# Performance work log

Hardware: AMD Instinct MI355X
Metric: run time of the kernel (lower is better)

## Reference

```python
import jax, jax.numpy as jnp
import numpy as np

H_DIM = 256
NUM_HEADS = 8
HEAD_DIM = H_DIM // NUM_HEADS
BN_EPS = 1e-5
SCALE = float(np.sqrt(HEAD_DIM))


def _lens():
    # 512 graphs, ragged vertex counts cycling 32/64/96/128 -> 40960 total rows
    return np.tile(np.array([32, 64, 96, 128], dtype=np.int64), 128)


def _pad(x, lens):
    # gather ragged rows of x [total, D] into padded [B, Lmax, D]; mask [B, Lmax]
    B = lens.shape[0]
    L = int(lens.max())
    off = np.zeros(B, np.int64)
    off[1:] = np.cumsum(lens)[:-1]
    pos = np.arange(L)
    idx = off[:, None] + np.minimum(pos[None, :], lens[:, None] - 1)
    mask = pos[None, :] < lens[:, None]
    return x[jnp.asarray(idx)], jnp.asarray(mask)


def _flat_idx(lens):
    # (graph_id, position) for every real row, to un-pad back to ragged layout
    b = np.repeat(np.arange(lens.shape[0]), lens)
    i = np.concatenate([np.arange(int(l)) for l in lens])
    return jnp.asarray(b), jnp.asarray(i)


def _forward(src_h, dst_h, src_lens, dst_lens,
             W1, b1, gamma1, beta1, W2, b2, gamma2, beta2):
    src_pad, src_mask = _pad(src_h, src_lens)   # [B, Ls, H]
    dst_pad, _ = _pad(dst_h, dst_lens)          # [B, Ld, H]
    B, Ls, _ = src_pad.shape
    Ld = dst_pad.shape[1]
    # NOTE: original torch code zips self.proj but never applies it, so
    # q = raw dst, k = v = raw src.  The .view(1, head_dim, heads, N) on the
    # channel-major tensor splits feature f as f = d*NUM_HEADS + h.
    q = dst_pad.reshape(B, Ld, HEAD_DIM, NUM_HEADS)
    k = src_pad.reshape(B, Ls, HEAD_DIM, NUM_HEADS)
    v = k
    scores = jnp.einsum('bndh,bmdh->bhnm', q, k) / SCALE
    scores = jnp.where(src_mask[:, None, None, :], scores, jnp.float32(-1e30))
    attn = jax.nn.softmax(scores, axis=-1)
    out = jnp.einsum('bhnm,bmdh->bndh', attn, v).reshape(B, Ld, H_DIM)
    bidx, iidx = _flat_idx(dst_lens)
    h_msg = out[bidx, iidx]                     # [total_dst, H] ragged again
    h = dst_h
    z = jnp.concatenate([h, h_msg], axis=-1)    # [N, 2H]
    y = z @ W1.T + b1
    y = gamma1 * (y - y.mean(0)) * jax.lax.rsqrt(y.var(0) + BN_EPS) + beta1
    y = jax.nn.relu(y)
    y = y @ W2.T + b2
    y = gamma2 * (y - y.mean(0)) * jax.lax.rsqrt(y.var(0) + BN_EPS) + beta2
    return h + y


def setup_inputs() -> dict:
    lens = _lens()
    N = int(lens.sum())
    ks = jax.random.split(jax.random.key(0), 4)
    return {
        'src_h': jax.random.normal(ks[0], (N, H_DIM), jnp.float32),
        'dst_h': jax.random.normal(ks[1], (N, H_DIM), jnp.float32),
        'src_num_verts': jnp.asarray(lens, jnp.int32),
        'dst_num_verts': jnp.asarray(lens, jnp.int32),
        'W1': jax.random.normal(ks[2], (H_DIM, 2 * H_DIM), jnp.float32) / np.float32(np.sqrt(2 * H_DIM)),
        'b1': jnp.zeros((H_DIM,), jnp.float32),
        'gamma1': jnp.ones((H_DIM,), jnp.float32),
        'beta1': jnp.zeros((H_DIM,), jnp.float32),
        'W2': jax.random.normal(ks[3], (H_DIM, H_DIM), jnp.float32) / np.float32(np.sqrt(H_DIM)),
        'b2': jnp.zeros((H_DIM,), jnp.float32),
        'gamma2': jnp.ones((H_DIM,), jnp.float32),
        'beta2': jnp.zeros((H_DIM,), jnp.float32),
    }


def reference(src_h, dst_h, src_num_verts, dst_num_verts,
              W1, b1, gamma1, beta1, W2, b2, gamma2, beta2):
    # segment lengths are static metadata (torch.split takes a Python list)
    src_lens = np.asarray(jax.device_get(src_num_verts), np.int64)
    dst_lens = np.asarray(jax.device_get(dst_num_verts), np.int64)
    return _forward(src_h, dst_h, src_lens, dst_lens,
                    W1, b1, gamma1, beta1, W2, b2, gamma2, beta2)
```

## Files before the change

### kernel.cpp

```cpp
#include <hip/hip_runtime.h>
#include <cstddef>

#define H 256
#define NHEADS 8
#define HD 32

typedef __attribute__((ext_vector_type(8))) short bf16x8;
typedef __attribute__((ext_vector_type(4))) float f32x4;

__device__ __forceinline__ float bf2f(unsigned short s) {
    unsigned u = ((unsigned)s) << 16; return __builtin_bit_cast(float, u);
}
__device__ __forceinline__ float bfe2f(short s) {
    unsigned u = ((unsigned)(unsigned short)s) << 16; return __builtin_bit_cast(float, u);
}
__device__ __forceinline__ unsigned short f2bf(float x) {
    unsigned u = __builtin_bit_cast(unsigned, x);
    u += 0x7fffu + ((u >> 16) & 1u);
    return (unsigned short)(u >> 16);
}
__device__ __forceinline__ void gl_lds16(const void* g, void* l) {
    __builtin_amdgcn_global_load_lds(
        (const __attribute__((address_space(1))) void*)g,
        (__attribute__((address_space(3))) void*)l, 16, 0, 0);
}

#define PS 2696
__global__ __launch_bounds__(256) void pre_kernel(
    const float* __restrict__ src, const float* __restrict__ dst,
    const float* __restrict__ W1, const float* __restrict__ W2,
    const int* __restrict__ slen, const int* __restrict__ dlen,
    unsigned short* __restrict__ KT, unsigned short* __restrict__ QT,
    unsigned short* __restrict__ W1p, unsigned short* __restrict__ W2bf,
    int* __restrict__ soff, int* __restrict__ doff,
    float* __restrict__ stats, int N, int B)
{
    __shared__ unsigned short pl[8 * PS];
    const int t = threadIdx.x;
    const int bid = blockIdx.x;
    const int prepB = N >> 5;

    if (bid < prepB) {
        const int rb = (bid >> 1) * 64;
        const int isrc = (bid & 1) == 0;
        const float* __restrict__ in = isrc ? src : dst;
        unsigned short* __restrict__ T = isrc ? KT : QT;
        #pragma unroll
        for (int i = 0; i < 16; ++i) {
            const int idx = t + i * 256;
            const int row = idx >> 6, f4 = idx & 63;
            const float4 v = ((const float4*)in)[(size_t)(rb + row) * 64 + f4];
            const int f0 = f4 * 4, h0 = f0 & 7, d = f0 >> 3;
            pl[(h0 + 0) * PS + row * 42 + d] = f2bf(v.x);
            pl[(h0 + 1) * PS + row * 42 + d] = f2bf(v.y);
            pl[(h0 + 2) * PS + row * 42 + d] = f2bf(v.z);
            pl[(h0 + 3) * PS + row * 42 + d] = f2bf(v.w);
        }
        __syncthreads();
        #pragma unroll
        for (int i = 0; i < 8; ++i) {
            const int idx = t + i * 256;
            const int h = idx >> 8, rem = idx & 255, row = rem >> 2, c = rem & 3;
            const bf16x8 val = *(const bf16x8*)&pl[h * PS + row * 42 + c * 8];
            *(bf16x8*)&T[(size_t)(h * N + rb + row) * 32 + c * 8] = val;
        }
    } else if (bid < prepB + 768) {
        const int idx = (bid - prepB) * 256 + t;
        if (idx < 131072) {
            const int kp = idx & 511, c = idx >> 9;
            const int half = kp >> 8, r = kp & 255, hh = r >> 5, d = r & 31;
            W1p[(size_t)c * 512 + kp] = f2bf(W1[(size_t)c * 512 + half * 256 + d * 8 + hh]);
        } else {
            const int i2 = idx - 131072;
            W2bf[i2] = f2bf(W2[i2]);
        }
    } else {
        stats[t] = 0.f; stats[t + 256] = 0.f; stats[t + 512] = 0.f; stats[t + 768] = 0.f;
        if (t < 64) {
            int sv[8], dv[8];
            int sl = 0, dl = 0;
            #pragma unroll
            for (int j = 0; j < 8; ++j) {
                const int g = t * 8 + j;
                sv[j] = sl; dv[j] = dl;
                sl += (g < B) ? slen[g] : 0;
                dl += (g < B) ? dlen[g] : 0;
            }
            int sx = sl, dx = dl;
            #pragma unroll
            for (int o = 1; o < 64; o <<= 1) {
                const int sy = __shfl_up(sx, o);
                const int dy = __shfl_up(dx, o);
                if (t >= o) { sx += sy; dx += dy; }
            }
            const int sbase = sx - sl, dbase = dx - dl;
            #pragma unroll
            for (int j = 0; j < 8; ++j) {
                const int g = t * 8 + j;
                if (g < B) { soff[g] = sbase + sv[j]; doff[g] = dbase + dv[j]; }
            }
        }
    }
}

template<int LS>
__device__ __forceinline__ void attn_body(
    const unsigned short* __restrict__ KT, const unsigned short* __restrict__ QT,
    unsigned short* __restrict__ OT,
    unsigned short* __restrict__ Ps, int N, int so, int df, int Ld, int h, int lane)
{
    constexpr int MT = LS / 16, CH = LS / 32;
    const int lr = lane & 15, lq = lane >> 4;
    const float iscale = 0.17677669529663687f;

    bf16x8 kf[MT];
    #pragma unroll
    for (int mt = 0; mt < MT; ++mt)
        kf[mt] = *(const bf16x8*)&KT[(size_t)(h * N + so + mt * 16 + lr) * 32 + lq * 8];

    bf16x8 vf[CH][2];
    #pragma unroll
    for (int c = 0; c < CH; ++c) {
        #pragma unroll
        for (int hf = 0; hf < 2; ++hf) {
            const bf16x8 kv = kf[2 * c + hf];
            const int nn = hf * 16 + lr;
            #pragma unroll
            for (int k = 0; k < 8; ++k)
                Ps[(lq * 8 + k) * 33 + nn] = (unsigned short)kv[k];
        }
        __asm__ volatile("" ::: "memory");
        __builtin_amdgcn_wave_barrier();
        #pragma unroll
        for (int dt = 0; dt < 2; ++dt)
            vf[c][dt] = *(const bf16x8*)&Ps[(dt * 16 + lr) * 33 + lq * 8];
        __asm__ volatile("" ::: "memory");
        __builtin_amdgcn_wave_barrier();
    }

    const int NT = Ld >> 4;
    bf16x8 qf = *(const bf16x8*)&QT[(size_t)(h * N + df + lr) * 32 + lq * 8];
    for (int nt = 0; nt < NT; ++nt) {
        bf16x8 qn = qf;
        if (nt + 1 < NT)
            qn = *(const bf16x8*)&QT[(size_t)(h * N + df + (nt + 1) * 16 + lr) * 32 + lq * 8];
        f32x4 s[MT];
        __builtin_amdgcn_s_setprio(1);
        #pragma unroll
        for (int mt = 0; mt < MT; ++mt) {
            f32x4 z = {0.f, 0.f, 0.f, 0.f};
            s[mt] = __builtin_amdgcn_mfma_f32_16x16x32_bf16(kf[mt], qf, z, 0, 0, 0);
        }
        __builtin_amdgcn_s_setprio(0);
        float mx = -INFINITY;
        #pragma unroll
        for (int mt = 0; mt < MT; ++mt)
            mx = fmaxf(mx, fmaxf(fmaxf(s[mt][0], s[mt][1]), fmaxf(s[mt][2], s[mt][3])));
        mx = fmaxf(mx, __shfl_xor(mx, 16));
        mx = fmaxf(mx, __shfl_xor(mx, 32));
        const float mxi = mx * iscale;
        float sum = 0.f;
        #pragma unroll
        for (int mt = 0; mt < MT; ++mt) {
            #pragma unroll
            for (int r = 0; r < 4; ++r) {
                const float e = __expf(s[mt][r] * iscale - mxi);
                s[mt][r] = e; sum += e;
            }
        }
        sum += __shfl_xor(sum, 16);
        sum += __shfl_xor(sum, 32);
        const float rinv = 1.f / sum;
        #pragma unroll
        for (int mt = 0; mt < MT; ++mt) {
            uint2 p;
            p.x = ((unsigned)f2bf(s[mt][0])) | (((unsigned)f2bf(s[mt][1])) << 16);
            p.y = ((unsigned)f2bf(s[mt][2])) | (((unsigned)f2bf(s[mt][3])) << 16);
            *(uint2*)&Ps[lr * 136 + mt * 16 + lq * 4] = p;
        }
        __asm__ volatile("" ::: "memory");
        __builtin_amdgcn_wave_barrier();
        f32x4 o0 = {0.f, 0.f, 0.f, 0.f}, o1 = {0.f, 0.f, 0.f, 0.f};
        __builtin_amdgcn_s_setprio(1);
        #pragma unroll
        for (int c = 0; c < CH; ++c) {
            const bf16x8 pa = *(const bf16x8*)&Ps[lr * 136 + c * 32 + lq * 8];
            o0 = __builtin_amdgcn_mfma_f32_16x16x32_bf16(pa, vf[c][0], o0, 0, 0, 0);
            o1 = __builtin_amdgcn_mfma_f32_16x16x32_bf16(pa, vf[c][1], o1, 0, 0, 0);
        }
        __builtin_amdgcn_s_setprio(0);
        __asm__ volatile("" ::: "memory");
        __builtin_amdgcn_wave_barrier();
        #pragma unroll
        for (int r = 0; r < 4; ++r) {
            const float rv = __shfl(rinv, lq * 4 + r);
            const int row = df + nt * 16 + lq * 4 + r;
            OT[(size_t)(h * N + row) * 32 + lr]      = f2bf(o0[r] * rv);
            OT[(size_t)(h * N + row) * 32 + 16 + lr] = f2bf(o1[r] * rv);
        }
        qf = qn;
    }
}

__global__ __launch_bounds__(256) void attn_mfma(
    const unsigned short* __restrict__ KT, const unsigned short* __restrict__ QT,
    unsigned short* __restrict__ OT,
    const int* __restrict__ soff, const int* __restrict__ doff,
    const int* __restrict__ slen, const int* __restrict__ dlen, int N)
{
    __shared__ unsigned short Ps[4][16 * 136];
    const int i = blockIdx.x >> 1, half = blockIdx.x & 1;
    const int grp = i >> 7, j = i & 127;
    const int b = 4 * j + (3 - grp);
    const int w = threadIdx.x >> 6, lane = threadIdx.x & 63;
    const int h = half * 4 + w;
    const int Ls = slen[b], Ld = dlen[b], so = soff[b], df = doff[b];
    switch (Ls) {
        case 32:  attn_body<32> (KT, QT, OT, Ps[w], N, so, df, Ld, h, lane); break;
        case 64:  attn_body<64> (KT, QT, OT, Ps[w], N, so, df, Ld, h, lane); break;
        case 96:  attn_body<96> (KT, QT, OT, Ps[w], N, so, df, Ld, h, lane); break;
        default:  attn_body<128>(KT, QT, OT, Ps[w], N, so, df, Ld, h, lane); break;
    }
}

__global__ __launch_bounds__(256) void gemm1_mfma(
    const unsigned short* __restrict__ QT, const unsigned short* __restrict__ OT,
    const unsigned short* __restrict__ W, const float* __restrict__ bias,
    unsigned short* __restrict__ out, float* __restrict__ sum, float* __restrict__ sq,
    int N)
{
    __shared__ unsigned short Abuf[2][8 * 512];
    __shared__ unsigned short Bbuf[2][8 * 512];
    const int tid = threadIdx.x;
    const int w = tid >> 6, lane = tid & 63;
    const int bid = blockIdx.x;
    const int xcd = bid & 7, q = bid >> 3;
    const int cb = q & 1, y = (q >> 1) * 8 + xcd;
    const int rowBase = y * 128, colBase = cb * 128;
    const int lr = lane & 15, lq = lane >> 4;
    const int wm = w >> 1, wn = w & 1;

    f32x4 acc[4][4];
    #pragma unroll
    for (int i = 0; i < 4; ++i)
        #pragma unroll
        for (int j = 0; j < 4; ++j) { f32x4 z = {0.f, 0.f, 0.f, 0.f}; acc[i][j] = z; }

    auto stage = [&](int ks, int bi) {
        const unsigned short* __restrict__ Ap = (ks < 8) ? QT : OT;
        const int hh = ks & 7;
        #pragma unroll
        for (int s = 0; s < 2; ++s) {
            const int sub = 2 * w + s;
            gl_lds16(Ap + (size_t)(hh * N + rowBase + sub * 16 + lr) * 32 + lq * 8,
                     &Abuf[bi][sub * 512]);
            gl_lds16(W + (size_t)(colBase + sub * 16 + lr) * 512 + ks * 32 + lq * 8,
                     &Bbuf[bi][sub * 512]);
        }
    };
    auto compute = [&](int bi) {
        bf16x8 af[4], bfr[4];
        #pragma unroll
        for (int i = 0; i < 4; ++i) af[i] = *(const bf16x8*)&Abuf[bi][(wm * 4 + i) * 512 + lane * 8];
        #pragma unroll
        for (int j = 0; j < 4; ++j) bfr[j] = *(const bf16x8*)&Bbuf[bi][(wn * 4 + j) * 512 + lane * 8];
        #pragma unroll
        for (int i = 0; i < 4; ++i)
            #pragma unroll
            for (int j = 0; j < 4; ++j)
                acc[i][j] = __builtin_amdgcn_mfma_f32_16x16x32_bf16(af[i], bfr[j], acc[i][j], 0, 0, 0);
    };

    stage(0, 0);
    __syncthreads();
    for (int ks = 0; ks < 16; ks += 2) {
        stage(ks + 1, 1);
        compute(0);
        __syncthreads();
        if (ks + 2 < 16) stage(ks + 2, 0);
        compute(1);
        __syncthreads();
    }

    const int col0 = colBase + wn * 64;
    #pragma unroll
    for (int j = 0; j < 4; ++j) {
        const int col = col0 + j * 16 + lr;
        const float bv = bias[col];
        float cs = 0.f, cq = 0.f;
        #pragma unroll
        for (int i = 0; i < 4; ++i) {
            const int row0 = rowBase + wm * 64 + i * 16 + lq * 4;
            #pragma unroll
            for (int r = 0; r < 4; ++r) {
                const float v = acc[i][j][r] + bv;
                cs += v; cq += v * v;
                out[(size_t)(row0 + r) * 256 + col] = f2bf(v);
            }
        }
        cs += __shfl_xor(cs, 16); cs += __shfl_xor(cs, 32);
        cq += __shfl_xor(cq, 16); cq += __shfl_xor(cq, 32);
        if (lq == 0) { atomicAdd(&sum[col], cs); atomicAdd(&sq[col], cq); }
    }
}

__global__ __launch_bounds__(256) void gemm2_fused(
    const unsigned short* __restrict__ y1,
    const unsigned short* __restrict__ W, const float* __restrict__ bias,
    const float* __restrict__ sum1, const float* __restrict__ sq1,
    const float* __restrict__ gamma1, const float* __restrict__ beta1,
    unsigned short* __restrict__ out, float* __restrict__ sum, float* __restrict__ sq,
    float invN)
{
    __shared__ unsigned short Abuf[2][8 * 512];
    __shared__ unsigned short Bbuf[2][8 * 512];
    __shared__ float scs[256], shs[256];
    const int tid = threadIdx.x;
    const int w = tid >> 6, lane = tid & 63;
    const int bid = blockIdx.x;
    const int xcd = bid & 7, q = bid >> 3;
    const int cb = q & 1, y = (q >> 1) * 8 + xcd;
    const int rowBase = y * 128, colBase = cb * 128;
    const int lr = lane & 15, lq = lane >> 4;
    const int wm = w >> 1, wn = w & 1;

    {
        const float mean = sum1[tid] * invN;
        const float var  = sq1[tid] * invN - mean * mean;
        const float rstd = rsqrtf(var + 1e-5f);
        const float sc = gamma1[tid] * rstd;
        scs[tid] = sc;
        shs[tid] = beta1[tid] - mean * sc;
    }

    f32x4 acc[4][4];
    #pragma unroll
    for (int i = 0; i < 4; ++i)
        #pragma unroll
        for (int j = 0; j < 4; ++j) { f32x4 z = {0.f, 0.f, 0.f, 0.f}; acc[i][j] = z; }

    bf16x8 rawA[2];
    auto loadA = [&](int ks) {
        #pragma unroll
        for (int s = 0; s < 2; ++s) {
            const int sub = 2 * w + s;
            rawA[s] = *(const bf16x8*)&y1[(size_t)(rowBase + sub * 16 + lr) * 256 + ks * 32 + lq * 8];
        }
    };
    auto writeA = [&](int ks, int bi) {
        const int k0 = ks * 32 + lq * 8;
        #pragma unroll
        for (int s = 0; s < 2; ++s) {
            const int sub = 2 * w + s;
            bf16x8 o;
            #pragma unroll
            for (int j = 0; j < 8; ++j)
                o[j] = (short)f2bf(fmaxf(bfe2f(rawA[s][j]) * scs[k0 + j] + shs[k0 + j], 0.f));
            *(bf16x8*)&Abuf[bi][sub * 512 + lane * 8] = o;
        }
    };
    auto stageB = [&](int ks, int bi) {
        #pragma unroll
        for (int s = 0; s < 2; ++s) {
            const int sub = 2 * w + s;
            gl_lds16(W + (size_t)(colBase + sub * 16 + lr) * 256 + ks * 32 + lq * 8,
                     &Bbuf[bi][sub * 512]);
        }
    };
    auto compute = [&](int bi) {
        bf16x8 af[4], bfr[4];
        #pragma unroll
        for (int i = 0; i < 4; ++i) af[i] = *(const bf16x8*)&Abuf[bi][(wm * 4 + i) * 512 + lane * 8];
        #pragma unroll
        for (int j = 0; j < 4; ++j) bfr[j] = *(const bf16x8*)&Bbuf[bi][(wn * 4 + j) * 512 + lane * 8];
        #pragma unroll
        for (int i = 0; i < 4; ++i)
            #pragma unroll
            for (int j = 0; j < 4; ++j)
                acc[i][j] = __builtin_amdgcn_mfma_f32_16x16x32_bf16(af[i], bfr[j], acc[i][j], 0, 0, 0);
    };

    __syncthreads();
    loadA(0); stageB(0, 0); writeA(0, 0);
    __syncthreads();
    for (int ks = 0; ks < 8; ++ks) {
        const int cur = ks & 1;
        if (ks + 1 < 8) { loadA(ks + 1); stageB(ks + 1, cur ^ 1); }
        compute(cur);
        if (ks + 1 < 8) writeA(ks + 1, cur ^ 1);
        __syncthreads();
    }

    const int col0 = colBase + wn * 64;
    #pragma unroll
    for (int j = 0; j < 4; ++j) {
        const int col = col0 + j * 16 + lr;
        const float bv = bias[col];
        float cs = 0.f, cq = 0.f;
        #pragma unroll
        for (int i = 0; i < 4; ++i) {
            const int row0 = rowBase + wm * 64 + i * 16 + lq * 4;
            #pragma unroll
            for (int r = 0; r < 4; ++r) {
                const float v = acc[i][j][r] + bv;
                cs += v; cq += v * v;
                out[(size_t)(row0 + r) * 256 + col] = f2bf(v);
            }
        }
        cs += __shfl_xor(cs, 16); cs += __shfl_xor(cs, 32);
        cq += __shfl_xor(cq, 16); cq += __shfl_xor(cq, 32);
        if (lq == 0) { atomicAdd(&sum[col], cs); atomicAdd(&sq[col], cq); }
    }
}

__global__ __launch_bounds__(256) void epilogue_kernel(
    const float* __restrict__ dst, const unsigned short* __restrict__ y2,
    const float* __restrict__ sum, const float* __restrict__ sq,
    const float* __restrict__ gamma, const float* __restrict__ beta,
    float* __restrict__ out, int n8, float invN)
{
    const int i = blockIdx.x * 256 + threadIdx.x;
    if (i >= n8) return;
    const int j0 = (i & 31) * 8;
    const bf16x8 yv = ((const bf16x8*)y2)[i];
    const float4 d0 = ((const float4*)dst)[2 * i];
    const float4 d1 = ((const float4*)dst)[2 * i + 1];
    float o[8];
    const float dv[8] = {d0.x, d0.y, d0.z, d0.w, d1.x, d1.y, d1.z, d1.w};
    #pragma unroll
    for (int j = 0; j < 8; ++j) {
        const float mean = sum[j0 + j] * invN;
        const float var  = sq[j0 + j] * invN - mean * mean;
        const float rstd = rsqrtf(var + 1e-5f);
        const float sc = gamma[j0 + j] * rstd;
        const float sh = beta[j0 + j] - mean * sc;
        o[j] = dv[j] + bfe2f(yv[j]) * sc + sh;
    }
    float4 o0, o1;
    o0.x = o[0]; o0.y = o[1]; o0.z = o[2]; o0.w = o[3];
    o1.x = o[4]; o1.y = o[5]; o1.z = o[6]; o1.w = o[7];
    ((float4*)out)[2 * i]     = o0;
    ((float4*)out)[2 * i + 1] = o1;
}

extern "C" void kernel_launch(void* const* d_in, const int* in_sizes, int n_in,
                              void* d_out, int out_size, void* d_ws, size_t ws_size,
                              hipStream_t stream)
{
    const float* src_h  = (const float*)d_in[0];
    const float* dst_h  = (const float*)d_in[1];
    const int*   slen   = (const int*)d_in[2];
    const int*   dlen   = (const int*)d_in[3];
    const float* W1     = (const float*)d_in[4];
    const float* b1     = (const float*)d_in[5];
    const float* gamma1 = (const float*)d_in[6];
    const float* beta1  = (const float*)d_in[7];
    const float* W2     = (const float*)d_in[8];
    const float* b2     = (const float*)d_in[9];
    const float* gamma2 = (const float*)d_in[10];
    const float* beta2  = (const float*)d_in[11];
    float* out = (float*)d_out;

    const int N = in_sizes[1] / H;
    const int B = in_sizes[2];

    char* base = (char*)d_ws;
    int*   soff   = (int*)(base + 0);
    int*   doff   = (int*)(base + 2048);
    float* stats  = (float*)(base + 4096);
    unsigned short* W1p  = (unsigned short*)(base + 16384);
    unsigned short* W2bf = (unsigned short*)(base + 16384 + 262144);
    const size_t S = (size_t)N * H * sizeof(unsigned short);
    char* big = base + (1 << 20);
    unsigned short* KT  = (unsigned short*)(big);
    unsigned short* QT  = (unsigned short*)(big + 2 * S);
    unsigned short* OT  = (unsigned short*)(big + 3 * S);
    unsigned short* y1bf = KT;
    unsigned short* y2bf = QT;

    const float invN = 1.0f / (float)N;

    const int prepB = N >> 5;
    pre_kernel<<<prepB + 768 + 1, 256, 0, stream>>>(
        src_h, dst_h, W1, W2, slen, dlen,
        KT, QT, W1p, W2bf, soff, doff, stats, N, B);

    attn_mfma<<<B * 2, 256, 0, stream>>>(KT, QT, OT, soff, doff, slen, dlen, N);

    gemm1_mfma<<<640, 256, 0, stream>>>(QT, OT, W1p, b1, y1bf, stats + 0, stats + 256, N);

    gemm2_fused<<<640, 256, 0, stream>>>(
        y1bf, W2bf, b2, stats + 0, stats + 256, gamma1, beta1,
        y2bf, stats + 512, stats + 768, invN);

    const int n8 = N * H / 8;
    epilogue_kernel<<<(n8 + 255) / 256, 256, 0, stream>>>(
        dst_h, y2bf, stats + 512, stats + 768, gamma2, beta2, out, n8, invN);
}
```

Baseline: 243.5 us.

## Split gemm1 K loop across two warp groups with LDS reduction

Doubles gemm1's block to 512 threads and gives each group of four waves half of the K dimension: one group handles the dst/Q half and the other the message/OT half. Each group runs its own double-buffered 8-step loop, and the partial accumulators are then summed through shared memory before the bias, BN statistics and store epilogue. The aim is to halve the serial K-loop length per block and raise the number of waves in flight. The cost is 64 KB of LDS per block, an extra LDS reduction round-trip, and possibly fewer resident blocks per CU.

```diff
diff --git a/kernel.cpp b/kernel.cpp
--- a/kernel.cpp
+++ b/kernel.cpp
@@ -223,22 +223,22 @@
     }
 }
 
-__global__ __launch_bounds__(256) void gemm1_mfma(
+__global__ __launch_bounds__(512) void gemm1_mfma(
     const unsigned short* __restrict__ QT, const unsigned short* __restrict__ OT,
     const unsigned short* __restrict__ W, const float* __restrict__ bias,
     unsigned short* __restrict__ out, float* __restrict__ sum, float* __restrict__ sq,
     int N)
 {
-    __shared__ unsigned short Abuf[2][8 * 512];
-    __shared__ unsigned short Bbuf[2][8 * 512];
+    __shared__ unsigned short LB[32768];
     const int tid = threadIdx.x;
     const int w = tid >> 6, lane = tid & 63;
+    const int kg = w >> 2, wq = w & 3;
+    const int wm = wq >> 1, wn = wq & 1;
     const int bid = blockIdx.x;
     const int xcd = bid & 7, q = bid >> 3;
     const int cb = q & 1, y = (q >> 1) * 8 + xcd;
     const int rowBase = y * 128, colBase = cb * 128;
     const int lr = lane & 15, lq = lane >> 4;
-    const int wm = w >> 1, wn = w & 1;
 
     f32x4 acc[4][4];
     #pragma unroll
@@ -246,24 +246,29 @@
         #pragma unroll
         for (int j = 0; j < 4; ++j) { f32x4 z = {0.f, 0.f, 0.f, 0.f}; acc[i][j] = z; }
 
-    auto stage = [&](int ks, int bi) {
+    auto stage = [&](int t, int bi) {
+        const int ks = kg * 8 + t;
         const unsigned short* __restrict__ Ap = (ks < 8) ? QT : OT;
         const int hh = ks & 7;
+        unsigned short* Ab = LB + kg * 8192 + bi * 4096;
+        unsigned short* Bb = LB + 16384 + kg * 8192 + bi * 4096;
         #pragma unroll
         for (int s = 0; s < 2; ++s) {
-            const int sub = 2 * w + s;
+            const int sub = 2 * wq + s;
             gl_lds16(Ap + (size_t)(hh * N + rowBase + sub * 16 + lr) * 32 + lq * 8,
-                     &Abuf[bi][sub * 512]);
+                     Ab + sub * 512);
             gl_lds16(W + (size_t)(colBase + sub * 16 + lr) * 512 + ks * 32 + lq * 8,
-                     &Bbuf[bi][sub * 512]);
+                     Bb + sub * 512);
         }
     };
     auto compute = [&](int bi) {
+        const unsigned short* Ab = LB + kg * 8192 + bi * 4096;
+        const unsigned short* Bb = LB + 16384 + kg * 8192 + bi * 4096;
         bf16x8 af[4], bfr[4];
         #pragma unroll
-        for (int i = 0; i < 4; ++i) af[i] = *(const bf16x8*)&Abuf[bi][(wm * 4 + i) * 512 + lane * 8];
-        #pragma unroll
-        for (int j = 0; j < 4; ++j) bfr[j] = *(const bf16x8*)&Bbuf[bi][(wn * 4 + j) * 512 + lane * 8];
+        for (int i = 0; i < 4; ++i) af[i] = *(const bf16x8*)&Ab[(wm * 4 + i) * 512 + lane * 8];
+        #pragma unroll
+        for (int j = 0; j < 4; ++j) bfr[j] = *(const bf16x8*)&Bb[(wn * 4 + j) * 512 + lane * 8];
         #pragma unroll
         for (int i = 0; i < 4; ++i)
             #pragma unroll
@@ -273,34 +278,56 @@
 
     stage(0, 0);
     __syncthreads();
-    for (int ks = 0; ks < 16; ks += 2) {
-        stage(ks + 1, 1);
+    for (int t = 0; t < 8; t += 2) {
+        stage(t + 1, 1);
         compute(0);
         __syncthreads();
-        if (ks + 2 < 16) stage(ks + 2, 0);
+        if (t + 2 < 8) stage(t + 2, 0);
         compute(1);
         __syncthreads();
     }
 
-    const int col0 = colBase + wn * 64;
-    #pragma unroll
-    for (int j = 0; j < 4; ++j) {
-        const int col = col0 + j * 16 + lr;
-        const float bv = bias[col];
-        float cs = 0.f, cq = 0.f;
-        #pragma unroll
-        for (int i = 0; i < 4; ++i) {
-            const int row0 = rowBase + wm * 64 + i * 16 + lq * 4;
-            #pragma unroll
-            for (int r = 0; r < 4; ++r) {
-                const float v = acc[i][j][r] + bv;
-                cs += v; cq += v * v;
-                out[(size_t)(row0 + r) * 256 + col] = f2bf(v);
+    float* red = (float*)LB;
+    if (tid >= 256) {
+        const int b0 = tid - 256;
+        #pragma unroll
+        for (int i = 0; i < 4; ++i)
+            #pragma unroll
+            for (int j = 0; j < 4; ++j)
+                #pragma unroll
+                for (int r = 0; r < 4; ++r)
+                    red[(((i * 4 + j) * 4) + r) * 256 + b0] = acc[i][j][r];
+    }
+    __syncthreads();
+    if (tid < 256) {
+        #pragma unroll
+        for (int i = 0; i < 4; ++i)
+            #pragma unroll
+            for (int j = 0; j < 4; ++j)
+                #pragma unroll
+                for (int r = 0; r < 4; ++r)
+                    acc[i][j][r] += red[(((i * 4 + j) * 4) + r) * 256 + tid];
+
+        const int col0 = colBase + wn * 64;
+        #pragma unroll
+        for (int j = 0; j < 4; ++j) {
+            const int col = col0 + j * 16 + lr;
+            const float bv = bias[col];
+            float cs = 0.f, cq = 0.f;
+            #pragma unroll
+            for (int i = 0; i < 4; ++i) {
+                const int row0 = rowBase + wm * 64 + i * 16 + lq * 4;
+                #pragma unroll
+                for (int r = 0; r < 4; ++r) {
+                    const float v = acc[i][j][r] + bv;
+                    cs += v; cq += v * v;
+                    out[(size_t)(row0 + r) * 256 + col] = f2bf(v);
+                }
             }
-        }
-        cs += __shfl_xor(cs, 16); cs += __shfl_xor(cs, 32);
-        cq += __shfl_xor(cq, 16); cq += __shfl_xor(cq, 32);
-        if (lq == 0) { atomicAdd(&sum[col], cs); atomicAdd(&sq[col], cq); }
+            cs += __shfl_xor(cs, 16); cs += __shfl_xor(cs, 32);
+            cq += __shfl_xor(cq, 16); cq += __shfl_xor(cq, 32);
+            if (lq == 0) { atomicAdd(&sum[col], cs); atomicAdd(&sq[col], cq); }
+        }
     }
 }
 
@@ -487,7 +514,7 @@
 
     attn_mfma<<<B * 2, 256, 0, stream>>>(KT, QT, OT, soff, doff, slen, dlen, N);
 
-    gemm1_mfma<<<640, 256, 0, stream>>>(QT, OT, W1p, b1, y1bf, stats + 0, stats + 256, N);
+    gemm1_mfma<<<640, 512, 0, stream>>>(QT, OT, W1p, b1, y1bf, stats + 0, stats + 256, N);
 
     gemm2_fused<<<640, 256, 0, stream>>>(
         y1bf, W2bf, b2, stats + 0, stats + 256, gamma1, beta1,
```

Measured after the change: 245.4 us. Within noise of the previous version (+0.8%).
